# Performance work log

Hardware: AMD Instinct MI355X
Metric: run time of the kernel (lower is better)

The kernel has to match this reference:

```python
import jax, jax.numpy as jnp
import numpy as np

NEG = -1e4      # BigBird additive mask value
LN_EPS = 1e-12  # BERT-style LayerNorm eps


def _bigbird_forward(xs_pad, mask, Wq, bq, Wk, bk, Wv, bv, Wo, bo, gamma, beta, rand_idx):
    b, n, hsz = xs_pad.shape
    H = rand_idx.shape[0]
    nb = rand_idx.shape[1] + 2          # one rand row per non-edge query block
    BS = n // nb                        # block size
    d = hsz // H
    r = rand_idx.shape[2]
    scale = 1.0 / np.sqrt(d).astype(np.float32)

    mf = mask.reshape(b, n).astype(xs_pad.dtype)   # (b,n) 1=token, 0=pad
    mb = mf.reshape(b, nb, BS)                     # blocked mask

    def proj(W, bias):
        return (xs_pad @ W + bias).reshape(b, n, H, d).transpose(0, 2, 1, 3)

    q = proj(Wq, bq) * scale            # (b,H,n,d)
    k = proj(Wk, bk)
    v = proj(Wv, bv)
    qb = q.reshape(b, H, nb, BS, d)
    kb = k.reshape(b, H, nb, BS, d)
    vb = v.reshape(b, H, nb, BS, d)

    # ---- global rows: first / last query block attend to all keys ----
    def full_row(qi):                   # qi: (b,H,BS,d)
        s = jnp.einsum('bhqd,bhkd->bhqk', qi, k) + (1.0 - mf)[:, None, None, :] * NEG
        return jnp.einsum('bhqk,bhkd->bhqd', jax.nn.softmax(s, axis=-1), v)

    ctx_first = full_row(qb[:, :, 0])
    ctx_last = full_row(qb[:, :, nb - 1])

    # ---- random key/value blocks: per-head, per-query-block gather ----
    hidx = jnp.arange(H)[:, None, None]
    rand_k = kb[:, hidx, rand_idx].reshape(b, H, nb - 2, r * BS, d)
    rand_v = vb[:, hidx, rand_idx].reshape(b, H, nb - 2, r * BS, d)
    rand_m = mb[:, rand_idx].reshape(b, H, nb - 2, r * BS)

    def sparse_row(qi, kc, vc, mc):     # kc:(b,H,K,d), mc:(b,H,K)
        s = jnp.einsum('bhqd,bhkd->bhqk', qi, kc) + (1.0 - mc)[:, :, None, :] * NEG
        return jnp.einsum('bhqk,bhkd->bhqd', jax.nn.softmax(s, axis=-1), vc)

    def gather_blocks(ids, ridx):
        kc = jnp.concatenate([kb[:, :, j] for j in ids] + [rand_k[:, :, ridx]], axis=2)
        vc = jnp.concatenate([vb[:, :, j] for j in ids] + [rand_v[:, :, ridx]], axis=2)
        mc = jnp.concatenate([jnp.broadcast_to(mb[:, None, j], (b, H, BS)) for j in ids]
                             + [rand_m[:, :, ridx]], axis=2)
        return kc, vc, mc

    # second / penultimate query blocks: window + globals + rand
    ctx_second = sparse_row(qb[:, :, 1], *gather_blocks([0, 1, 2, nb - 1], 0))
    ctx_penult = sparse_row(qb[:, :, nb - 2], *gather_blocks([nb - 3, nb - 2, nb - 1, 0], nb - 3))

    # ---- middle rows i in [2, nb-3]: 3-block sliding window + first/last global + r random ----
    nmid = nb - 4
    mid = jnp.arange(2, nb - 2)
    win = mid[:, None] + jnp.arange(-1, 2)[None, :]        # (nmid,3)
    k_win = kb[:, :, win].reshape(b, H, nmid, 3 * BS, d)
    v_win = vb[:, :, win].reshape(b, H, nmid, 3 * BS, d)
    m_win = jnp.broadcast_to(mb[:, win].reshape(b, 1, nmid, 3 * BS), (b, H, nmid, 3 * BS))

    def rep_glob(t):                     # (b,H,BS,...) -> (b,H,nmid,BS,...)
        return jnp.broadcast_to(t[:, :, None], (b, H, nmid) + t.shape[2:])

    k_mid = jnp.concatenate([k_win, rep_glob(kb[:, :, 0]), rep_glob(kb[:, :, nb - 1]),
                             rand_k[:, :, 1:nb - 3]], axis=3)
    v_mid = jnp.concatenate([v_win, rep_glob(vb[:, :, 0]), rep_glob(vb[:, :, nb - 1]),
                             rand_v[:, :, 1:nb - 3]], axis=3)
    m_first = jnp.broadcast_to(mb[:, None, None, 0], (b, H, nmid, BS))
    m_last = jnp.broadcast_to(mb[:, None, None, nb - 1], (b, H, nmid, BS))
    m_mid = jnp.concatenate([m_win, m_first, m_last, rand_m[:, :, 1:nb - 3]], axis=3)

    s_mid = jnp.einsum('bhmqd,bhmkd->bhmqk', qb[:, :, 2:nb - 2], k_mid) \
            + (1.0 - m_mid)[:, :, :, None, :] * NEG
    ctx_mid = jnp.einsum('bhmqk,bhmkd->bhmqd', jax.nn.softmax(s_mid, axis=-1), v_mid)

    ctx = jnp.concatenate([ctx_first[:, :, None], ctx_second[:, :, None], ctx_mid,
                           ctx_penult[:, :, None], ctx_last[:, :, None]], axis=2)
    ctx = ctx.reshape(b, H, n, d).transpose(0, 2, 1, 3).reshape(b, n, hsz)
    ctx = ctx * mf[:, :, None]           # from_mask on output rows

    # BigBirdSelfOutput: dense + residual + LayerNorm (dropout=0 / eval)
    y = ctx @ Wo + bo + xs_pad
    mu = y.mean(-1, keepdims=True)
    var = ((y - mu) ** 2).mean(-1, keepdims=True)
    return (y - mu) * jax.lax.rsqrt(var + LN_EPS) * gamma + beta


def setup_inputs() -> dict:
    key = jax.random.key(0)
    ks = jax.random.split(key, 6)
    B, N, HSZ, H, BS, R = 4, 4096, 1024, 16, 64, 3
    NB = N // BS
    init = lambda k, shp: jax.random.normal(k, shp, dtype=jnp.float32) * 0.02
    return {
        'xs_pad': jax.random.normal(ks[0], (B, N, HSZ), dtype=jnp.float32),
        'mask': jnp.ones((B, 1, N), dtype=jnp.int32),
        'Wq': init(ks[1], (HSZ, HSZ)), 'bq': jnp.zeros((HSZ,), jnp.float32),
        'Wk': init(ks[2], (HSZ, HSZ)), 'bk': jnp.zeros((HSZ,), jnp.float32),
        'Wv': init(ks[3], (HSZ, HSZ)), 'bv': jnp.zeros((HSZ,), jnp.float32),
        'Wo': init(ks[4], (HSZ, HSZ)), 'bo': jnp.zeros((HSZ,), jnp.float32),
        'gamma': jnp.ones((HSZ,), jnp.float32), 'beta': jnp.zeros((HSZ,), jnp.float32),
        'rand_idx': jax.random.randint(ks[5], (H, NB - 2, R), 1, NB - 1).astype(jnp.int32),
    }


def reference(xs_pad, mask, Wq, bq, Wk, bk, Wv, bv, Wo, bo, gamma, beta, rand_idx):
    return _bigbird_forward(xs_pad, mask, Wq, bq, Wk, bk, Wv, bv, Wo, bo, gamma, beta, rand_idx)
```

## Files before the change

### kernel.cpp

```cpp
#include <hip/hip_runtime.h>
#include <hip/hip_bf16.h>

#define B_   4
#define N_   4096
#define HSZ  1024
#define H_   16
#define D_   64
#define NB_  64
#define R_   3
#define M_   (B_*N_)
#define NEGV (-1e4f)
#define LOG2E 1.4426950408889634f

typedef float f32x4 __attribute__((ext_vector_type(4)));
typedef short s16x8 __attribute__((ext_vector_type(8)));
typedef __bf16 b16x8 __attribute__((ext_vector_type(8)));

__device__ __forceinline__ f32x4 mfma16(s16x8 a, s16x8 b, f32x4 c) {
  return __builtin_amdgcn_mfma_f32_16x16x32_bf16(
      __builtin_bit_cast(b16x8, a), __builtin_bit_cast(b16x8, b), c, 0, 0, 0);
}

__device__ __forceinline__ short f2b(float x) {
  __hip_bfloat16 h = __float2bfloat16(x);
  return (short)__builtin_bit_cast(unsigned short, h);
}

__device__ __forceinline__ unsigned pack2(float a, float b) {
  return (unsigned)(unsigned short)f2b(a) |
         ((unsigned)(unsigned short)f2b(b) << 16);
}

__device__ __forceinline__ void gl_lds16(const short* g, short* l) {
  __builtin_amdgcn_global_load_lds(
      (const __attribute__((address_space(1))) unsigned int*)g,
      (__attribute__((address_space(3))) unsigned int*)l, 16, 0, 0);
}

__global__ __launch_bounds__(256) void k_prep(const float* __restrict__ in,
                                              short* __restrict__ out,
                                              const float* __restrict__ Wq,
                                              const float* __restrict__ Wk,
                                              const float* __restrict__ Wv,
                                              const float* __restrict__ Wo,
                                              short* __restrict__ wt) {
  const int tid = threadIdx.x;
  if (blockIdx.x < 8192) {
    size_t i = ((size_t)blockIdx.x * 256 + tid) * 8;
    float4 a = *(const float4*)&in[i];
    float4 b = *(const float4*)&in[i + 4];
    s16x8 o;
    o[0] = f2b(a.x); o[1] = f2b(a.y); o[2] = f2b(a.z); o[3] = f2b(a.w);
    o[4] = f2b(b.x); o[5] = f2b(b.y); o[6] = f2b(b.z); o[7] = f2b(b.w);
    *(s16x8*)&out[i] = o;
    return;
  }
  const int bid = blockIdx.x - 8192;
  const int z = bid >> 8;
  const int rest = bid & 255;
  const int tk = (rest >> 4) * 64, tn = (rest & 15) * 64;
  const float* src = (z == 0) ? Wq : (z == 1) ? Wk : (z == 2) ? Wv : Wo;
  short* dst = wt + (size_t)z * HSZ * HSZ;
  __shared__ __align__(16) float t[64][68];
#pragma unroll
  for (int r = 0; r < 4; ++r) {
    int c = tid + r * 256;
    int row = c >> 4, seg = c & 15;
    *(float4*)&t[row][seg * 4] =
        *(const float4*)&src[(size_t)(tk + row) * HSZ + tn + seg * 4];
  }
  __syncthreads();
#pragma unroll
  for (int r = 0; r < 2; ++r) {
    int c = tid + r * 256;
    int row = c >> 3, seg = c & 7;
    s16x8 o;
#pragma unroll
    for (int u = 0; u < 8; ++u) o[u] = f2b(t[seg * 8 + u][row]);
    *(s16x8*)&dst[(size_t)(tn + row) * HSZ + tk + seg * 8] = o;
  }
}

template <bool SWAP>
__device__ __forceinline__ void gemm_core(
    const short* __restrict__ A, const short* __restrict__ Bt, int tm, int tn,
    short (&a_lds)[2][128][64], short (&b_lds)[2][128][64],
    f32x4 (&acc)[4][4], int wave, int lane) {
  const int lq = lane & 15, g = lane >> 4;
  const int wm = (wave & 1) * 64, wn = (wave >> 1) * 64;
  const int srow = wave * 32 + (lane >> 3);
  const int scol = ((lane & 7) ^ ((lane >> 3) & 7)) * 8;

  auto STAGE = [&](int buf, int kt) {
#pragma unroll
    for (int u = 0; u < 4; ++u) {
      gl_lds16(&A[(size_t)(tm + srow + u * 8) * HSZ + kt + scol],
               &a_lds[buf][wave * 32 + u * 8][0]);
      gl_lds16(&Bt[(size_t)(tn + srow + u * 8) * HSZ + kt + scol],
               &b_lds[buf][wave * 32 + u * 8][0]);
    }
  };

  const int sw = (lq & 7) << 3;
  auto COMPUTE = [&](int buf) {
#pragma unroll
    for (int kk = 0; kk < 2; ++kk) {
      const int ko = (kk * 32 + g * 8) ^ sw;
      s16x8 af[4], bf[4];
#pragma unroll
      for (int i = 0; i < 4; ++i)
        af[i] = *(const s16x8*)&a_lds[buf][wm + i * 16 + lq][ko];
#pragma unroll
      for (int j = 0; j < 4; ++j)
        bf[j] = *(const s16x8*)&b_lds[buf][wn + j * 16 + lq][ko];
#pragma unroll
      for (int i = 0; i < 4; ++i)
#pragma unroll
        for (int j = 0; j < 4; ++j)
          acc[i][j] = SWAP ? mfma16(bf[j], af[i], acc[i][j])
                           : mfma16(af[i], bf[j], acc[i][j]);
    }
  };

  STAGE(0, 0);
  STAGE(1, 64);
  int cur = 0;
  for (int s2 = 0; s2 < 14; ++s2) {
    asm volatile("s_waitcnt vmcnt(8)" ::: "memory");
    __builtin_amdgcn_s_barrier();
    COMPUTE(cur);
    __builtin_amdgcn_s_barrier();
    STAGE(cur, (s2 + 2) * 64);
    cur ^= 1;
  }
  asm volatile("s_waitcnt vmcnt(8)" ::: "memory");
  __builtin_amdgcn_s_barrier();
  COMPUTE(cur);
  cur ^= 1;
  asm volatile("s_waitcnt vmcnt(0)" ::: "memory");
  __builtin_amdgcn_s_barrier();
  COMPUTE(cur);
}

__global__ __launch_bounds__(256) void k_qkv(
    const short* __restrict__ A, const short* __restrict__ WT,
    const float* __restrict__ bq, const float* __restrict__ bk,
    const float* __restrict__ bv, short* __restrict__ oq,
    short* __restrict__ ok, short* __restrict__ ovt) {
  const int orig = blockIdx.x;
  const int xcd = orig & 7, r = orig >> 3;
  const int tml = r / 24, rem = r % 24;
  const int z = rem >> 3, tnl = rem & 7;
  const int tm = (xcd * 16 + tml) * 128, tn = tnl * 128;
  const short* Bt = WT + (size_t)z * HSZ * HSZ;

  __shared__ __align__(16) short a_lds[2][128][64];
  __shared__ __align__(16) short b_lds[2][128][64];

  const int tid = threadIdx.x, lane = tid & 63, wave = tid >> 6;
  const int lq = lane & 15, g = lane >> 4;
  const int wm = (wave & 1) * 64, wn = (wave >> 1) * 64;

  f32x4 acc[4][4] = {};

  if (z == 2) {
    gemm_core<false>(A, Bt, tm, tn, a_lds, b_lds, acc, wave, lane);
#pragma unroll
    for (int j = 0; j < 4; ++j) {
      const int col = tn + wn + j * 16 + lq;
      const int hh = col >> 6, dd = col & 63;
      const float bi = bv[col];
#pragma unroll
      for (int i = 0; i < 4; ++i) {
        const int nrow = tm + wm + i * 16 + g * 4;
        const int bb = nrow >> 12, nn = nrow & (N_ - 1);
        uint2 w;
        w.x = pack2(acc[i][j][0] + bi, acc[i][j][1] + bi);
        w.y = pack2(acc[i][j][2] + bi, acc[i][j][3] + bi);
        *(uint2*)&ovt[(((size_t)bb * H_ + hh) * D_ + dd) * N_ + nn] = w;
      }
    }
  } else {
    gemm_core<true>(A, Bt, tm, tn, a_lds, b_lds, acc, wave, lane);
    const float* bias = z ? bk : bq;
    short* outb = z ? ok : oq;
    const float alpha = z ? 1.0f : 0.125f * LOG2E;
#pragma unroll
    for (int i = 0; i < 4; ++i) {
      const int row = tm + wm + i * 16 + lq;
#pragma unroll
      for (int j = 0; j < 4; ++j) {
        const int colb = tn + wn + j * 16 + g * 4;
        const float4 bi = *(const float4*)&bias[colb];
        const int bb = row >> 12, nn = row & (N_ - 1);
        const int hh = colb >> 6, dd = colb & 63;
        uint2 w;
        w.x = pack2((acc[i][j][0] + bi.x) * alpha,
                    (acc[i][j][1] + bi.y) * alpha);
        w.y = pack2((acc[i][j][2] + bi.z) * alpha,
                    (acc[i][j][3] + bi.w) * alpha);
        *(uint2*)&outb[(((size_t)bb * H_ + hh) * N_ + nn) * D_ + dd] = w;
      }
    }
  }
}

__global__ __launch_bounds__(256) void k_out(
    const short* __restrict__ A, const short* __restrict__ WT,
    const float* __restrict__ bo, const float* __restrict__ xs,
    float* __restrict__ yout) {
  const short* Bt = WT + (size_t)3 * HSZ * HSZ;

  __shared__ __align__(16) short a_lds[2][128][64];
  __shared__ __align__(16) short b_lds[2][128][64];

  const int tid = threadIdx.x, lane = tid & 63, wave = tid >> 6;
  const int lq = lane & 15, g = lane >> 4;
  const int wm = (wave & 1) * 64, wn = (wave >> 1) * 64;
  const int orig = blockIdx.x;
  const int swg = (orig & 7) * 128 + (orig >> 3);
  const int tm = (swg >> 3) * 128, tn = (swg & 7) * 128;

  f32x4 acc[4][4] = {};
  gemm_core<true>(A, Bt, tm, tn, a_lds, b_lds, acc, wave, lane);

#pragma unroll
  for (int i = 0; i < 4; ++i) {
    const int row = tm + wm + i * 16 + lq;
#pragma unroll
    for (int j = 0; j < 4; ++j) {
      const int colb = tn + wn + j * 16 + g * 4;
      const float4 bi = *(const float4*)&bo[colb];
      const size_t idx = (size_t)row * HSZ + colb;
      const float4 xv = *(const float4*)&xs[idx];
      float4 yv;
      yv.x = acc[i][j][0] + bi.x + xv.x;
      yv.y = acc[i][j][1] + bi.y + xv.y;
      yv.z = acc[i][j][2] + bi.z + xv.z;
      yv.w = acc[i][j][3] + bi.w + xv.w;
      *(float4*)&yout[idx] = yv;
    }
  }
}

__global__ __launch_bounds__(256) void k_attn(
    const short* __restrict__ Q, const short* __restrict__ K,
    const short* __restrict__ VT, const int* __restrict__ mask,
    const int* __restrict__ rnd, short* __restrict__ ctx,
    float* __restrict__ pO, float* __restrict__ pm, float* __restrict__ pl) {
  const int orig = blockIdx.x;
  const int swg = (orig & 7) * 624 + (orig >> 3);
  const int s = swg % 78;
  const int bh_i = swg / 78;
  const int h = bh_i & 15, b = bh_i >> 4;
  const int tid = threadIdx.x, lane = tid & 63, wave = tid >> 6;
  const int g = lane >> 4, lq = lane & 15;

  __shared__ __align__(16) short k_lds[64][64];
  __shared__ __align__(16) short vt_lds[64][64];
  __shared__ __align__(16) short p_lds[4][16][72];
  __shared__ __align__(16) float bias_s[8][64];
  __shared__ int list_s[8];
  __shared__ int Ls;

  const bool mid = (s < 62);
  const int qb = mid ? (s + 1) : (((s - 62) >> 3) ? (NB_ - 1) : 0);

  if (tid == 0) {
    int L;
    if (!mid) {
      int chunk = (s - 62) & 7;
#pragma unroll
      for (int i = 0; i < 8; ++i) list_s[i] = chunk * 8 + i;
      L = 8;
    } else {
      const int* rp = rnd + ((size_t)h * (NB_ - 2) + (qb - 1)) * R_;
      int n;
      if (qb == 1) {
        list_s[0] = 0; list_s[1] = 1; list_s[2] = 2; list_s[3] = NB_ - 1; n = 4;
      } else if (qb == NB_ - 2) {
        list_s[0] = NB_ - 3; list_s[1] = NB_ - 2; list_s[2] = NB_ - 1;
        list_s[3] = 0; n = 4;
      } else {
        list_s[0] = qb - 1; list_s[1] = qb; list_s[2] = qb + 1;
        list_s[3] = 0; list_s[4] = NB_ - 1; n = 5;
      }
      for (int j = 0; j < R_; ++j) list_s[n + j] = rp[j];
      L = n + R_;
      for (int i = L; i < 8; ++i) list_s[i] = 0;
    }
    Ls = L;
  }

  const size_t bh = (size_t)b * H_ + h;
  const size_t qrow = bh * N_ + (size_t)qb * 64 + wave * 16 + lq;
  s16x8 qf0 = *(const s16x8*)&Q[qrow * D_ + g * 8];
  s16x8 qf1 = *(const s16x8*)&Q[qrow * D_ + 32 + g * 8];

  __syncthreads();
  const int L = Ls;

  const int r0 = tid >> 3, sg = tid & 7;
  const int csl = (sg ^ (r0 & 7)) * 8;
  const int sw = (lq & 7);

  const short* Kb = K + bh * (size_t)N_ * D_;
  const short* Vb = VT + bh * (size_t)D_ * N_;
  const int* mb = mask + (size_t)b * N_;

  for (int t = tid; t < 512; t += 256) {
    const int i = t >> 6, kk2 = t & 63;
    bias_s[i][kk2] =
        (1.0f - (float)mb[list_s[i] * 64 + kk2]) * (NEGV * LOG2E);
  }

  s16x8 kr0, kr1, vr0, vr1;
  {
    const int kb = list_s[0];
    const short* kp = Kb + (size_t)kb * 64 * D_;
    const short* vp = Vb + (size_t)kb * 64;
    kr0 = *(const s16x8*)&kp[(size_t)r0 * D_ + sg * 8];
    kr1 = *(const s16x8*)&kp[(size_t)(r0 + 32) * D_ + sg * 8];
    vr0 = *(const s16x8*)&vp[(size_t)r0 * N_ + sg * 8];
    vr1 = *(const s16x8*)&vp[(size_t)(r0 + 32) * N_ + sg * 8];
  }

  s16x8 ones;
#pragma unroll
  for (int u = 0; u < 8; ++u) ones[u] = (short)0x3F80;

  f32x4 o[4] = {};
  f32x4 osum = {};
  float mshift = 0.0f;

  for (int it = 0; it < L; ++it) {
    *(s16x8*)&k_lds[r0][csl] = kr0;
    *(s16x8*)&k_lds[r0 + 32][csl] = kr1;
    *(s16x8*)&vt_lds[r0][csl] = vr0;
    *(s16x8*)&vt_lds[r0 + 32][csl] = vr1;
    if (it + 1 < L) {
      const int kb = list_s[it + 1];
      const short* kp = Kb + (size_t)kb * 64 * D_;
      const short* vp = Vb + (size_t)kb * 64;
      kr0 = *(const s16x8*)&kp[(size_t)r0 * D_ + sg * 8];
      kr1 = *(const s16x8*)&kp[(size_t)(r0 + 32) * D_ + sg * 8];
      vr0 = *(const s16x8*)&vp[(size_t)r0 * N_ + sg * 8];
      vr1 = *(const s16x8*)&vp[(size_t)(r0 + 32) * N_ + sg * 8];
    }
    __syncthreads();

    f32x4 st[4];
#pragma unroll
    for (int f = 0; f < 4; ++f) {
      f32x4 a0 = *(const f32x4*)&bias_s[it][f * 16 + g * 4];
      s16x8 af0 = *(const s16x8*)&k_lds[f * 16 + lq][(g ^ sw) * 8];
      s16x8 af1 = *(const s16x8*)&k_lds[f * 16 + lq][((4 + g) ^ sw) * 8];
      a0 = mfma16(af0, qf0, a0);
      a0 = mfma16(af1, qf1, a0);
      st[f] = a0;
    }

    if (mshift == 0.0f) {
#pragma unroll
      for (int f = 0; f < 4; ++f)
#pragma unroll
        for (int e = 0; e < 4; ++e) st[f][e] = exp2f(st[f][e]);
    } else {
#pragma unroll
      for (int f = 0; f < 4; ++f)
#pragma unroll
        for (int e = 0; e < 4; ++e) st[f][e] = exp2f(st[f][e] - mshift);
    }

#pragma unroll
    for (int f = 0; f < 4; ++f) {
      uint2 w = make_uint2(pack2(st[f][0], st[f][1]),
                           pack2(st[f][2], st[f][3]));
      *(uint2*)&p_lds[wave][lq][f * 16 + g * 4] = w;
    }

#pragma unroll
    for (int kk = 0; kk < 2; ++kk) {
      s16x8 pa = *(const s16x8*)&p_lds[wave][lq][kk * 32 + g * 8];
#pragma unroll
      for (int j = 0; j < 4; ++j) {
        s16x8 bv =
            *(const s16x8*)&vt_lds[j * 16 + lq][((kk * 4 + g) ^ sw) * 8];
        o[j] = mfma16(pa, bv, o[j]);
      }
      osum = mfma16(pa, ones, osum);
    }

    float om = fmaxf(fmaxf(osum[0], osum[1]), fmaxf(osum[2], osum[3]));
    if (__any(om > 16777216.0f)) {
#pragma unroll
      for (int j = 0; j < 4; ++j) o[j] *= 5.9604645e-08f;
      osum *= 5.9604645e-08f;
      mshift += 24.0f;
    }
    __syncthreads();
  }

  if (mid) {
    float rs[4];
#pragma unroll
    for (int e = 0; e < 4; ++e)
      rs[e] = (float)mb[qb * 64 + wave * 16 + g * 4 + e] /
              fmaxf(osum[e], 1e-30f);
#pragma unroll
    for (int j = 0; j < 4; ++j) {
      k_lds[wave * 16 + g * 4 + 0][j * 16 + lq] = f2b(o[j][0] * rs[0]);
      k_lds[wave * 16 + g * 4 + 1][j * 16 + lq] = f2b(o[j][1] * rs[1]);
      k_lds[wave * 16 + g * 4 + 2][j * 16 + lq] = f2b(o[j][2] * rs[2]);
      k_lds[wave * 16 + g * 4 + 3][j * 16 + lq] = f2b(o[j][3] * rs[3]);
    }
    __syncthreads();
#pragma unroll
    for (int pp = 0; pp < 2; ++pp) {
      int c = tid + pp * 256;
      int row = c >> 3, seg = c & 7;
      *(s16x8*)&ctx[((size_t)b * N_ + qb * 64 + row) * HSZ + h * D_ + seg * 8] =
          *(const s16x8*)&k_lds[row][seg * 8];
    }
  } else {
    const int e2 = s - 62;
    const int qsel = e2 >> 3, chunk = e2 & 7;
    const size_t eidx = (bh * 2 + qsel) * 8 + chunk;
    float* po = pO + eidx * 4096;
#pragma unroll
    for (int j = 0; j < 4; ++j)
#pragma unroll
      for (int e = 0; e < 4; ++e)
        po[(wave * 16 + g * 4 + e) * 64 + j * 16 + lq] = o[j][e];
    if (lq == 0) {
#pragma unroll
      for (int e = 0; e < 4; ++e) {
        pm[eidx * 64 + wave * 16 + g * 4 + e] = mshift;
        pl[eidx * 64 + wave * 16 + g * 4 + e] = osum[e];
      }
    }
  }
}

__global__ __launch_bounds__(256) void k_comb(
    const float* __restrict__ pO, const float* __restrict__ pm,
    const float* __restrict__ pl, const int* __restrict__ mask,
    short* __restrict__ ctx) {
  const int qsel = blockIdx.x, h = blockIdx.y, b = blockIdx.z;
  const int qb = qsel ? NB_ - 1 : 0;
  const int tid = threadIdx.x;
  const int q = tid >> 2, dq = tid & 3;
  const size_t base = (((size_t)b * H_ + h) * 2 + qsel) * 8;

  float mv[8];
  float M = -INFINITY;
#pragma unroll
  for (int i = 0; i < 8; ++i) {
    mv[i] = pm[(base + i) * 64 + q];
    M = fmaxf(M, mv[i]);
  }
  float Lsum = 0.0f;
#pragma unroll
  for (int i = 0; i < 8; ++i) {
    float w = exp2f(mv[i] - M);
    mv[i] = w;
    Lsum += pl[(base + i) * 64 + q] * w;
  }
  f32x4 acc[4] = {};
#pragma unroll
  for (int i = 0; i < 8; ++i) {
    const float* p = pO + (base + i) * 4096 + q * 64 + dq * 16;
    float w = mv[i];
#pragma unroll
    for (int u = 0; u < 4; ++u) {
      f32x4 v = *(const f32x4*)&p[u * 4];
      acc[u] += v * w;
    }
  }
  float sc = (float)mask[(size_t)b * N_ + qb * 64 + q] / fmaxf(Lsum, 1e-30f);
  s16x8 out0, out1;
#pragma unroll
  for (int u = 0; u < 8; ++u) {
    out0[u] = f2b(acc[u >> 2][u & 3] * sc);
    out1[u] = f2b(acc[2 + (u >> 2)][u & 3] * sc);
  }
  short* dst = &ctx[((size_t)b * N_ + qb * 64 + q) * HSZ + h * D_ + dq * 16];
  *(s16x8*)dst = out0;
  *(s16x8*)(dst + 8) = out1;
}

__global__ __launch_bounds__(256) void k_ln(float* __restrict__ y,
                                            const float* __restrict__ gamma,
                                            const float* __restrict__ beta) {
  const int row = blockIdx.x, tid = threadIdx.x, lane = tid & 63,
            wave = tid >> 6;
  __shared__ float s_sum[4], s_sq[4];
  float4 v = *(const float4*)&y[(size_t)row * HSZ + tid * 4];
  float s = v.x + v.y + v.z + v.w;
  float q = v.x * v.x + v.y * v.y + v.z * v.z + v.w * v.w;
#pragma unroll
  for (int m = 1; m <= 32; m <<= 1) {
    s += __shfl_xor(s, m);
    q += __shfl_xor(q, m);
  }
  if (lane == 0) { s_sum[wave] = s; s_sq[wave] = q; }
  __syncthreads();
  float S = s_sum[0] + s_sum[1] + s_sum[2] + s_sum[3];
  float Qs = s_sq[0] + s_sq[1] + s_sq[2] + s_sq[3];
  float mu = S * (1.0f / HSZ);
  float var = Qs * (1.0f / HSZ) - mu * mu;
  float r = rsqrtf(var + 1e-12f);
  float4 g = *(const float4*)&gamma[tid * 4];
  float4 be = *(const float4*)&beta[tid * 4];
  float4 outv;
  outv.x = (v.x - mu) * r * g.x + be.x;
  outv.y = (v.y - mu) * r * g.y + be.y;
  outv.z = (v.z - mu) * r * g.z + be.z;
  outv.w = (v.w - mu) * r * g.w + be.w;
  *(float4*)&y[(size_t)row * HSZ + tid * 4] = outv;
}

extern "C" void kernel_launch(void* const* d_in, const int* in_sizes, int n_in,
                              void* d_out, int out_size, void* d_ws,
                              size_t ws_size, hipStream_t stream) {
  const float* xs = (const float*)d_in[0];
  const int* mask = (const int*)d_in[1];
  const float* Wq = (const float*)d_in[2];
  const float* bq = (const float*)d_in[3];
  const float* Wk = (const float*)d_in[4];
  const float* bk = (const float*)d_in[5];
  const float* Wv = (const float*)d_in[6];
  const float* bv = (const float*)d_in[7];
  const float* Wo = (const float*)d_in[8];
  const float* bo = (const float*)d_in[9];
  const float* gamma = (const float*)d_in[10];
  const float* beta = (const float*)d_in[11];
  const int* rnd = (const int*)d_in[12];
  float* yout = (float*)d_out;

  char* ws = (char*)d_ws;
  const size_t SZ_XS = (size_t)M_ * HSZ * 2;
  const size_t SZ_WT = (size_t)4 * HSZ * HSZ * 2;
  short* xsb = (short*)ws;
  short* wt = (short*)(ws + SZ_XS);
  short* qbuf = (short*)(ws + SZ_XS + SZ_WT);
  short* kbuf = qbuf + (size_t)M_ * HSZ;
  short* vtb = kbuf + (size_t)M_ * HSZ;
  char* after = ws + SZ_XS + SZ_WT + 3 * SZ_XS;
  float* pO = (float*)(after + (1 << 20));
  float* pm = pO + (size_t)1024 * 4096;
  float* pl = pm + (size_t)1024 * 64;

  k_prep<<<9216, 256, 0, stream>>>(xs, xsb, Wq, Wk, Wv, Wo, wt);
  k_qkv<<<3072, 256, 0, stream>>>(xsb, wt, bq, bk, bv, qbuf, kbuf, vtb);
  k_attn<<<4992, 256, 0, stream>>>(qbuf, kbuf, vtb, mask, rnd, xsb, pO, pm,
                                   pl);
  k_comb<<<dim3(2, H_, B_), 256, 0, stream>>>(pO, pm, pl, mask, xsb);
  k_out<<<1024, 256, 0, stream>>>(xsb, wt, bo, xs, yout);
  k_ln<<<M_, 256, 0, stream>>>(yout, gamma, beta);
}
```

Before: 343.7 us.

## Enlarge GEMM tiles to 256x256 with 8-wave blocks and interleaved staging

Replaces the 128x128, 4-wave GEMM core used by the QKV and output projections with a 256x256 tile computed by 8 waves. Each wave now holds 8x4 accumulators. Loads for the next K-slices are interleaved between compute phases, with per-phase barriers and setprio around the MFMA bursts. The goal is more data reuse per byte loaded and better overlap of global-to-LDS traffic with matrix math. The cost is 128KB of LDS per block and fewer blocks: 768 and 256, which gives only one wave of blocks for k_out on 256 CUs. That lowers occupancy and makes tail effects more likely.

```diff
diff --git a/kernel.cpp b/kernel.cpp
--- a/kernel.cpp
+++ b/kernel.cpp
@@ -82,97 +82,129 @@
 }
 
 template <bool SWAP>
-__device__ __forceinline__ void gemm_core(
+__device__ __forceinline__ void gemm8_core(
     const short* __restrict__ A, const short* __restrict__ Bt, int tm, int tn,
-    short (&a_lds)[2][128][64], short (&b_lds)[2][128][64],
-    f32x4 (&acc)[4][4], int wave, int lane) {
+    short (&a_lds)[2][256][64], short (&b_lds)[2][256][64],
+    f32x4 (&acc)[8][4], int wave, int lane) {
   const int lq = lane & 15, g = lane >> 4;
-  const int wm = (wave & 1) * 64, wn = (wave >> 1) * 64;
-  const int srow = wave * 32 + (lane >> 3);
-  const int scol = ((lane & 7) ^ ((lane >> 3) & 7)) * 8;
-
-  auto STAGE = [&](int buf, int kt) {
-#pragma unroll
-    for (int u = 0; u < 4; ++u) {
-      gl_lds16(&A[(size_t)(tm + srow + u * 8) * HSZ + kt + scol],
-               &a_lds[buf][wave * 32 + u * 8][0]);
-      gl_lds16(&Bt[(size_t)(tn + srow + u * 8) * HSZ + kt + scol],
-               &b_lds[buf][wave * 32 + u * 8][0]);
+  const int wm = wave >> 2, wn = wave & 3;
+  const int sl8 = lane >> 3;
+  const int sc = ((lane & 7) ^ sl8) * 8;
+
+  auto ST_A = [&](int buf, int kt, int h) {
+#pragma unroll
+    for (int u = 0; u < 2; ++u) {
+      const int rbase = h * 128 + wave * 8 + u * 64;
+      gl_lds16(&A[(size_t)(tm + rbase + sl8) * HSZ + kt * 64 + sc],
+               &a_lds[buf][rbase][0]);
     }
   };
-
-  const int sw = (lq & 7) << 3;
-  auto COMPUTE = [&](int buf) {
-#pragma unroll
-    for (int kk = 0; kk < 2; ++kk) {
-      const int ko = (kk * 32 + g * 8) ^ sw;
-      s16x8 af[4], bf[4];
-#pragma unroll
-      for (int i = 0; i < 4; ++i)
-        af[i] = *(const s16x8*)&a_lds[buf][wm + i * 16 + lq][ko];
+  auto ST_B = [&](int buf, int kt, int h) {
+#pragma unroll
+    for (int u = 0; u < 2; ++u) {
+      const int rbase = h * 128 + wave * 8 + u * 64;
+      gl_lds16(&Bt[(size_t)(tn + rbase + sl8) * HSZ + kt * 64 + sc],
+               &b_lds[buf][rbase][0]);
+    }
+  };
+
+  s16x8 bf[4][2];
+  auto LOADB = [&](int buf) {
+#pragma unroll
+    for (int j = 0; j < 4; ++j) {
+      const int row = wn * 64 + j * 16 + lq;
+#pragma unroll
+      for (int kk = 0; kk < 2; ++kk)
+        bf[j][kk] =
+            *(const s16x8*)&b_lds[buf][row][((kk * 4 + g) ^ (lq & 7)) * 8];
+    }
+  };
+  auto PH = [&](int buf, int m0) {
+    s16x8 af[2][2];
+#pragma unroll
+    for (int i = 0; i < 2; ++i) {
+      const int row = wm * 128 + (m0 + i) * 16 + lq;
+#pragma unroll
+      for (int kk = 0; kk < 2; ++kk)
+        af[i][kk] =
+            *(const s16x8*)&a_lds[buf][row][((kk * 4 + g) ^ (lq & 7)) * 8];
+    }
+    __builtin_amdgcn_s_setprio(1);
+#pragma unroll
+    for (int i = 0; i < 2; ++i)
 #pragma unroll
       for (int j = 0; j < 4; ++j)
-        bf[j] = *(const s16x8*)&b_lds[buf][wn + j * 16 + lq][ko];
-#pragma unroll
-      for (int i = 0; i < 4; ++i)
-#pragma unroll
-        for (int j = 0; j < 4; ++j)
-          acc[i][j] = SWAP ? mfma16(bf[j], af[i], acc[i][j])
-                           : mfma16(af[i], bf[j], acc[i][j]);
-    }
+#pragma unroll
+        for (int kk = 0; kk < 2; ++kk)
+          acc[m0 + i][j] = SWAP
+                               ? mfma16(bf[j][kk], af[i][kk], acc[m0 + i][j])
+                               : mfma16(af[i][kk], bf[j][kk], acc[m0 + i][j]);
+    __builtin_amdgcn_s_setprio(0);
+    __builtin_amdgcn_s_barrier();
   };
 
-  STAGE(0, 0);
-  STAGE(1, 64);
-  int cur = 0;
-  for (int s2 = 0; s2 < 14; ++s2) {
+  ST_A(0, 0, 0); ST_A(0, 0, 1);
+  ST_B(0, 0, 0); ST_B(0, 0, 1);
+  ST_B(1, 1, 0); ST_B(1, 1, 1);
+
+  for (int p = 0; p < 8; ++p) {
+    const int t = 2 * p;
+    ST_A(1, t + 1, 0); ST_A(1, t + 1, 1);
     asm volatile("s_waitcnt vmcnt(8)" ::: "memory");
     __builtin_amdgcn_s_barrier();
-    COMPUTE(cur);
+    LOADB(0);
+    PH(0, 0);
+    if (t + 2 < 16) { ST_B(0, t + 2, 0); ST_B(0, t + 2, 1); }
+    PH(0, 2);
+    PH(0, 4);
+    PH(0, 6);
+    if (t + 2 < 16) { ST_A(0, t + 2, 0); ST_A(0, t + 2, 1); }
+    if (p < 7) {
+      asm volatile("s_waitcnt vmcnt(8)" ::: "memory");
+    } else {
+      asm volatile("s_waitcnt vmcnt(0)" ::: "memory");
+    }
     __builtin_amdgcn_s_barrier();
-    STAGE(cur, (s2 + 2) * 64);
-    cur ^= 1;
-  }
-  asm volatile("s_waitcnt vmcnt(8)" ::: "memory");
-  __builtin_amdgcn_s_barrier();
-  COMPUTE(cur);
-  cur ^= 1;
-  asm volatile("s_waitcnt vmcnt(0)" ::: "memory");
-  __builtin_amdgcn_s_barrier();
-  COMPUTE(cur);
-}
-
-__global__ __launch_bounds__(256) void k_qkv(
+    LOADB(1);
+    PH(1, 0);
+    if (t + 3 < 16) { ST_B(1, t + 3, 0); ST_B(1, t + 3, 1); }
+    PH(1, 2);
+    PH(1, 4);
+    PH(1, 6);
+  }
+}
+
+__global__ __launch_bounds__(512, 2) void k_qkv(
     const short* __restrict__ A, const short* __restrict__ WT,
     const float* __restrict__ bq, const float* __restrict__ bk,
     const float* __restrict__ bv, short* __restrict__ oq,
     short* __restrict__ ok, short* __restrict__ ovt) {
   const int orig = blockIdx.x;
   const int xcd = orig & 7, r = orig >> 3;
-  const int tml = r / 24, rem = r % 24;
-  const int z = rem >> 3, tnl = rem & 7;
-  const int tm = (xcd * 16 + tml) * 128, tn = tnl * 128;
+  const int tml = r / 12, rem = r % 12;
+  const int z = rem >> 2, tnl = rem & 3;
+  const int tm = (xcd * 8 + tml) * 256, tn = tnl * 256;
   const short* Bt = WT + (size_t)z * HSZ * HSZ;
 
-  __shared__ __align__(16) short a_lds[2][128][64];
-  __shared__ __align__(16) short b_lds[2][128][64];
+  __shared__ __align__(16) short a_lds[2][256][64];
+  __shared__ __align__(16) short b_lds[2][256][64];
 
   const int tid = threadIdx.x, lane = tid & 63, wave = tid >> 6;
   const int lq = lane & 15, g = lane >> 4;
-  const int wm = (wave & 1) * 64, wn = (wave >> 1) * 64;
-
-  f32x4 acc[4][4] = {};
+  const int wm = wave >> 2, wn = wave & 3;
+
+  f32x4 acc[8][4] = {};
 
   if (z == 2) {
-    gemm_core<false>(A, Bt, tm, tn, a_lds, b_lds, acc, wave, lane);
+    gemm8_core<false>(A, Bt, tm, tn, a_lds, b_lds, acc, wave, lane);
 #pragma unroll
     for (int j = 0; j < 4; ++j) {
-      const int col = tn + wn + j * 16 + lq;
+      const int col = tn + wn * 64 + j * 16 + lq;
       const int hh = col >> 6, dd = col & 63;
       const float bi = bv[col];
 #pragma unroll
-      for (int i = 0; i < 4; ++i) {
-        const int nrow = tm + wm + i * 16 + g * 4;
+      for (int i = 0; i < 8; ++i) {
+        const int nrow = tm + wm * 128 + i * 16 + g * 4;
         const int bb = nrow >> 12, nn = nrow & (N_ - 1);
         uint2 w;
         w.x = pack2(acc[i][j][0] + bi, acc[i][j][1] + bi);
@@ -181,16 +213,16 @@
       }
     }
   } else {
-    gemm_core<true>(A, Bt, tm, tn, a_lds, b_lds, acc, wave, lane);
+    gemm8_core<true>(A, Bt, tm, tn, a_lds, b_lds, acc, wave, lane);
     const float* bias = z ? bk : bq;
     short* outb = z ? ok : oq;
     const float alpha = z ? 1.0f : 0.125f * LOG2E;
 #pragma unroll
-    for (int i = 0; i < 4; ++i) {
-      const int row = tm + wm + i * 16 + lq;
+    for (int i = 0; i < 8; ++i) {
+      const int row = tm + wm * 128 + i * 16 + lq;
 #pragma unroll
       for (int j = 0; j < 4; ++j) {
-        const int colb = tn + wn + j * 16 + g * 4;
+        const int colb = tn + wn * 64 + j * 16 + g * 4;
         const float4 bi = *(const float4*)&bias[colb];
         const int bb = row >> 12, nn = row & (N_ - 1);
         const int hh = colb >> 6, dd = colb & 63;
@@ -205,31 +237,32 @@
   }
 }
 
-__global__ __launch_bounds__(256) void k_out(
+__global__ __launch_bounds__(512, 2) void k_out(
     const short* __restrict__ A, const short* __restrict__ WT,
     const float* __restrict__ bo, const float* __restrict__ xs,
     float* __restrict__ yout) {
   const short* Bt = WT + (size_t)3 * HSZ * HSZ;
 
-  __shared__ __align__(16) short a_lds[2][128][64];
-  __shared__ __align__(16) short b_lds[2][128][64];
+  __shared__ __align__(16) short a_lds[2][256][64];
+  __shared__ __align__(16) short b_lds[2][256][64];
 
   const int tid = threadIdx.x, lane = tid & 63, wave = tid >> 6;
   const int lq = lane & 15, g = lane >> 4;
-  const int wm = (wave & 1) * 64, wn = (wave >> 1) * 64;
+  const int wm = wave >> 2, wn = wave & 3;
   const int orig = blockIdx.x;
-  const int swg = (orig & 7) * 128 + (orig >> 3);
-  const int tm = (swg >> 3) * 128, tn = (swg & 7) * 128;
-
-  f32x4 acc[4][4] = {};
-  gemm_core<true>(A, Bt, tm, tn, a_lds, b_lds, acc, wave, lane);
-
-#pragma unroll
-  for (int i = 0; i < 4; ++i) {
-    const int row = tm + wm + i * 16 + lq;
+  const int xcd = orig & 7, r = orig >> 3;
+  const int tml = r >> 2, tnl = r & 3;
+  const int tm = (xcd * 8 + tml) * 256, tn = tnl * 256;
+
+  f32x4 acc[8][4] = {};
+  gemm8_core<true>(A, Bt, tm, tn, a_lds, b_lds, acc, wave, lane);
+
+#pragma unroll
+  for (int i = 0; i < 8; ++i) {
+    const int row = tm + wm * 128 + i * 16 + lq;
 #pragma unroll
     for (int j = 0; j < 4; ++j) {
-      const int colb = tn + wn + j * 16 + g * 4;
+      const int colb = tn + wn * 64 + j * 16 + g * 4;
       const float4 bi = *(const float4*)&bo[colb];
       const size_t idx = (size_t)row * HSZ + colb;
       const float4 xv = *(const float4*)&xs[idx];
@@ -552,10 +585,10 @@
   float* pl = pm + (size_t)1024 * 64;
 
   k_prep<<<9216, 256, 0, stream>>>(xs, xsb, Wq, Wk, Wv, Wo, wt);
-  k_qkv<<<3072, 256, 0, stream>>>(xsb, wt, bq, bk, bv, qbuf, kbuf, vtb);
+  k_qkv<<<768, 512, 0, stream>>>(xsb, wt, bq, bk, bv, qbuf, kbuf, vtb);
   k_attn<<<4992, 256, 0, stream>>>(qbuf, kbuf, vtb, mask, rnd, xsb, pO, pm,
                                    pl);
   k_comb<<<dim3(2, H_, B_), 256, 0, stream>>>(pO, pm, pl, mask, xsb);
-  k_out<<<1024, 256, 0, stream>>>(xsb, wt, bo, xs, yout);
+  k_out<<<256, 512, 0, stream>>>(xsb, wt, bo, xs, yout);
   k_ln<<<M_, 256, 0, stream>>>(yout, gamma, beta);
 }
```

Result: faster. 325.4 us (-5.3%).
